# Performance work log

Hardware: AMD Instinct MI355X
Metric: run time of the kernel (lower is better)

The kernel has to match this reference:

```python
import jax, jax.numpy as jnp
import numpy as np

N = 2097152   # total points across all samples
B = 8         # number of point clouds in the batch
C = 64        # feature channels of fea


def setup_inputs() -> dict:
    key = jax.random.key(0)
    k1, k2, k3, k4 = jax.random.split(key, 4)
    fea = jax.random.normal(k1, (N, C), dtype=jnp.float32)
    pred_f = jax.random.normal(k2, (N, 1), dtype=jnp.float32)
    batch_ids = jnp.sort(jax.random.randint(k3, (N,), 0, B).astype(jnp.int32))
    target_points_num = jax.random.randint(k4, (B,), 0, 250000).astype(jnp.int32)
    return {"fea": fea, "pred_f": pred_f, "batch_ids": batch_ids,
            "target_points_num": target_points_num}


def reference(fea, pred_f, batch_ids, target_points_num):
    """BCE branch of GenerativeUpsample.get_keep + feature pruning.

    For each sample b with n_b points and target t_b: if n_b > t_b, threshold is the
    (n_b - t_b)-th smallest pred value (torch.kthvalue, 1-indexed), else dtype min.
    keep = pred > threshold[batch_id]; pruned fea = fea masked by keep.
    """
    vals = pred_f[:, 0]                                  # [N]
    n = vals.shape[0]
    counts = jax.ops.segment_sum(jnp.ones((n,), jnp.int32), batch_ids,
                                 num_segments=B)         # [B] points per sample
    offsets = jnp.concatenate([jnp.zeros((1,), jnp.int32),
                               jnp.cumsum(counts)[:-1].astype(jnp.int32)])
    pos = jnp.arange(n, dtype=jnp.int32) - offsets[batch_ids]  # index within segment

    # Pad each sample's values into a dense row (pad=+inf so pads sort to the end).
    dense = jnp.full((B, n), jnp.inf, dtype=vals.dtype).at[batch_ids, pos].set(vals)
    dense_sorted = jnp.sort(dense, axis=1)               # [B, N]

    # kth smallest (1-indexed k = n_b - t_b) -> sorted index n_b - t_b - 1.
    k_idx = jnp.clip(counts - target_points_num - 1, 0, n - 1)
    kth = jnp.take_along_axis(dense_sorted, k_idx[:, None].astype(jnp.int32), axis=1)[:, 0]
    thresh = jnp.where(counts > target_points_num, kth,
                       jnp.finfo(vals.dtype).min)        # [B]

    keep = vals > thresh[batch_ids]                      # [N] bool
    pruned_fea = fea * keep[:, None].astype(fea.dtype)   # [N, C]
    return pruned_fea, keep
```

## Files before the change

### kernel.cpp

```cpp
#include <hip/hip_runtime.h>
#include <float.h>


#define BATCHES 8

typedef float f32x4 __attribute__((ext_vector_type(4)));

__device__ __forceinline__ unsigned f2key(float x) {
    unsigned u = __float_as_uint(x);
    return (u & 0x80000000u) ? ~u : (u | 0x80000000u);
}
__device__ __forceinline__ float key2f(unsigned k) {
    unsigned u = (k & 0x80000000u) ? (k & 0x7FFFFFFFu) : ~k;
    return __uint_as_float(u);
}

__device__ unsigned g_hist[4 * BATCHES * 256];
__device__ unsigned g_remk[BATCHES];
__device__ unsigned g_prefix[BATCHES];
__device__ unsigned g_active[BATCHES];
__device__ float    g_thresh[BATCHES];

__global__ __launch_bounds__(256) void hist0_kernel(const float* __restrict__ pred,
                                                    const int* __restrict__ bids,
                                                    int n) {
    __shared__ unsigned lh[BATCHES * 256];
    for (int i = threadIdx.x; i < BATCHES * 256; i += 256) lh[i] = 0u;
    __syncthreads();
    int stride = gridDim.x * blockDim.x;
    for (int i = blockIdx.x * blockDim.x + threadIdx.x; i < n; i += stride) {
        int b = bids[i];
        unsigned key = f2key(pred[i]);
        atomicAdd(&lh[b * 256 + (key >> 24)], 1u);
    }
    __syncthreads();
    for (int i = threadIdx.x; i < BATCHES * 256; i += 256) {
        unsigned v = lh[i];
        if (v) atomicAdd(&g_hist[i], v);
    }
}

__global__ __launch_bounds__(256) void histN_kernel(const float* __restrict__ pred,
                                                    const int* __restrict__ bids,
                                                    int n, int shiftHi, int shiftBin,
                                                    int pass) {
    __shared__ unsigned lh[BATCHES * 256];
    __shared__ unsigned lpre[BATCHES];
    __shared__ unsigned lact[BATCHES];
    for (int i = threadIdx.x; i < BATCHES * 256; i += 256) lh[i] = 0u;
    if (threadIdx.x < BATCHES) {
        lpre[threadIdx.x] = g_prefix[threadIdx.x];
        lact[threadIdx.x] = g_active[threadIdx.x];
    }
    __syncthreads();
    int stride = gridDim.x * blockDim.x;
    for (int i = blockIdx.x * blockDim.x + threadIdx.x; i < n; i += stride) {
        int b = bids[i];
        if (!lact[b]) continue;
        unsigned key = f2key(pred[i]);
        if ((key >> shiftHi) == lpre[b])
            atomicAdd(&lh[b * 256 + ((key >> shiftBin) & 0xFFu)], 1u);
    }
    __syncthreads();
    unsigned* gh = g_hist + pass * BATCHES * 256;
    for (int i = threadIdx.x; i < BATCHES * 256; i += 256) {
        unsigned v = lh[i];
        if (v) atomicAdd(&gh[i], v);
    }
}

__global__ __launch_bounds__(256) void scan_kernel(const int* __restrict__ target,
                                                   int pass) {
    int b = blockIdx.x;
    int t = threadIdx.x;
    unsigned* h = g_hist + (pass * BATCHES + b) * 256;
    unsigned c = h[t];
    h[t] = 0u;
    if (pass > 0 && !g_active[b]) {
        if (pass == 3 && t == 0) g_thresh[b] = -FLT_MAX;
        return;
    }
    __shared__ unsigned s[256];
    s[t] = c;
    __syncthreads();
    for (int off = 1; off < 256; off <<= 1) {
        unsigned v = s[t];
        unsigned a = (t >= off) ? s[t - off] : 0u;
        __syncthreads();
        s[t] = v + a;
        __syncthreads();
    }
    unsigned incl = s[t];
    unsigned total = s[255];
    unsigned r;
    if (pass == 0) {
        int tg = target[b];
        bool act = ((int)total > tg) && (total > 0u);
        if (t == 0) g_active[b] = act ? 1u : 0u;
        if (!act) return;
        r = total - (unsigned)tg - 1u;
    } else {
        r = g_remk[b];
    }
    __syncthreads();
    unsigned excl = incl - c;
    if (c > 0u && excl <= r && r < incl) {
        unsigned p = (pass == 0) ? (unsigned)t : ((g_prefix[b] << 8) | (unsigned)t);
        g_prefix[b] = p;
        g_remk[b] = r - excl;
        if (pass == 3) g_thresh[b] = key2f(p);
    }
}

__global__ __launch_bounds__(256) void prune_kernel(const float* __restrict__ fea,
                                                    const float* __restrict__ pred,
                                                    const int* __restrict__ bids,
                                                    float* __restrict__ out,
                                                    int n) {
    __shared__ float sth[BATCHES];
    if (threadIdx.x < BATCHES) sth[threadIdx.x] = g_thresh[threadIdx.x];
    __syncthreads();
    long total4 = (long)n * 16;
    long stride = (long)gridDim.x * blockDim.x;
    for (long idx = (long)blockIdx.x * blockDim.x + threadIdx.x; idx < total4;
         idx += stride) {
        int row = (int)(idx >> 4);
        int l = (int)(idx & 15);
        int b = bids[row];
        bool kp = pred[row] > sth[b];
        f32x4 v = {0.f, 0.f, 0.f, 0.f};
        if (kp) v = __builtin_nontemporal_load((const f32x4*)fea + idx);
        __builtin_nontemporal_store(v, (f32x4*)out + idx);
        if (l == 0) {
            __builtin_nontemporal_store(kp ? 1.0f : 0.0f,
                                        out + (size_t)n * 64 + row);
        }
    }
}

extern "C" void kernel_launch(void* const* d_in, const int* in_sizes, int n_in,
                              void* d_out, int out_size, void* d_ws, size_t ws_size,
                              hipStream_t stream) {
    (void)d_ws; (void)ws_size; (void)n_in; (void)out_size;
    const float* fea    = (const float*)d_in[0];
    const float* pred   = (const float*)d_in[1];
    const int*   bids   = (const int*)d_in[2];
    const int*   target = (const int*)d_in[3];
    float* out = (float*)d_out;
    int n = in_sizes[1];

    hist0_kernel<<<1024, 256, 0, stream>>>(pred, bids, n);
    scan_kernel<<<BATCHES, 256, 0, stream>>>(target, 0);

    for (int p = 1; p <= 3; p++) {
        int shiftHi = 32 - 8 * p;
        int shiftBin = 24 - 8 * p;
        histN_kernel<<<2048, 256, 0, stream>>>(pred, bids, n, shiftHi, shiftBin, p);
        scan_kernel<<<BATCHES, 256, 0, stream>>>(target, p);
    }

    prune_kernel<<<8192, 256, 0, stream>>>(fea, pred, bids, out, n);
}
```

Measured before the change: 908.6 us.

## Fuse radix-select passes and pruning into one cooperative kernel with register-held keys

Replaces the nine-launch pipeline (histogram, scan, three refinement passes, prune) with a single cooperative kernel. Each thread loads its eight pred keys and batch ids once into registers and reuses them across all four radix passes. Grid-wide syncs replace kernel boundaries, and every block redundantly does the per-batch scans with wave shuffles. The trade is grid.sync overhead and a fixed 1024-block grid doing the bandwidth-bound feature copy, with the old path kept as a fallback if the cooperative launch fails.

```diff
diff --git a/kernel.cpp b/kernel.cpp
--- a/kernel.cpp
+++ b/kernel.cpp
@@ -1,8 +1,16 @@
 #include <hip/hip_runtime.h>
+#include <hip/hip_cooperative_groups.h>
 #include <float.h>
 
+namespace cg = cooperative_groups;
+
 
 #define BATCHES 8
+#define NBLK 1024
+#define NTHR 256
+#define NTOT (NBLK * NTHR)
+#define MAXE 8
+#define NEG_FLT_MAX_KEY 0x00800000u
 
 typedef float f32x4 __attribute__((ext_vector_type(4)));
 
@@ -21,6 +29,159 @@
 __device__ unsigned g_active[BATCHES];
 __device__ float    g_thresh[BATCHES];
 
+
+__global__ __launch_bounds__(NTHR, 4) void fused_kernel(
+        const float* __restrict__ fea,
+        const float* __restrict__ pred,
+        const int* __restrict__ bids,
+        const int* __restrict__ target,
+        float* __restrict__ out,
+        int n) {
+    cg::grid_group grid = cg::this_grid();
+    __shared__ unsigned lh[BATCHES * 256];
+    __shared__ unsigned lpre[BATCHES];
+    __shared__ unsigned lremk[BATCHES];
+    __shared__ unsigned lact[BATCHES];
+    __shared__ unsigned lthreshk[BATCHES];
+    __shared__ float    skeep[NTHR];
+
+    const int t = threadIdx.x;
+    const int tid = blockIdx.x * NTHR + t;
+
+    if (blockIdx.x == 0) {
+        for (int i = t; i < 4 * BATCHES * 256; i += NTHR) g_hist[i] = 0u;
+    }
+    for (int i = t; i < BATCHES * 256; i += NTHR) lh[i] = 0u;
+    __syncthreads();
+
+    unsigned key[MAXE];
+    unsigned bn = 0u;
+    #pragma unroll
+    for (int i = 0; i < MAXE; i++) {
+        int idx = tid + i * NTOT;
+        unsigned k = 0u, b = 8u;
+        if (idx < n) {
+            k = f2key(pred[idx]);
+            b = (unsigned)bids[idx];
+            atomicAdd(&lh[b * 256 + (k >> 24)], 1u);
+        }
+        key[i] = k;
+        bn |= (b << (4 * i));
+    }
+    __syncthreads();
+    grid.sync();
+
+    for (int i = t; i < BATCHES * 256; i += NTHR) {
+        unsigned v = lh[i];
+        if (v) atomicAdd(&g_hist[i], v);
+        lh[i] = 0u;
+    }
+    grid.sync();
+
+    #pragma unroll
+    for (int p = 0; p < 4; p++) {
+        {
+            int lane = t & 63;
+            int w = t >> 6;
+            for (int bb = 0; bb < 2; bb++) {
+                int b = w + bb * 4;
+                if (p > 0 && lact[b] == 0u) {
+                    if (p == 3 && lane == 0) lthreshk[b] = NEG_FLT_MAX_KEY;
+                    continue;
+                }
+                const unsigned* h = g_hist + (p * BATCHES + b) * 256;
+                unsigned c0 = h[lane * 4 + 0], c1 = h[lane * 4 + 1];
+                unsigned c2 = h[lane * 4 + 2], c3 = h[lane * 4 + 3];
+                unsigned lt = c0 + c1 + c2 + c3;
+                unsigned sc = lt;
+                #pragma unroll
+                for (int off = 1; off < 64; off <<= 1) {
+                    unsigned u = __shfl_up(sc, off);
+                    if (lane >= off) sc += u;
+                }
+                unsigned total = __shfl(sc, 63);
+                unsigned r;
+                if (p == 0) {
+                    int tg = target[b];
+                    bool act = ((int)total > tg);
+                    if (lane == 0) lact[b] = act ? 1u : 0u;
+                    if (!act) continue;
+                    r = total - (unsigned)tg - 1u;
+                } else {
+                    r = lremk[b];
+                }
+                unsigned excl = sc - lt;
+                if (r >= excl && r < sc) {
+                    unsigned rr = r - excl;
+                    unsigned bin, cum;
+                    if (rr < c0)                { bin = 0u; cum = 0u; }
+                    else if (rr < c0 + c1)      { bin = 1u; cum = c0; }
+                    else if (rr < c0 + c1 + c2) { bin = 2u; cum = c0 + c1; }
+                    else                        { bin = 3u; cum = c0 + c1 + c2; }
+                    unsigned binidx = (unsigned)(lane * 4) + bin;
+                    unsigned np = (p == 0) ? binidx : ((lpre[b] << 8) | binidx);
+                    lpre[b] = np;
+                    lremk[b] = rr - cum;
+                    if (p == 3) lthreshk[b] = np;
+                }
+            }
+        }
+        __syncthreads();
+
+        if (p == 3) break;
+
+        const int shiftHi  = 24 - 8 * p;
+        const int shiftBin = 16 - 8 * p;
+        #pragma unroll
+        for (int i = 0; i < MAXE; i++) {
+            unsigned b = (bn >> (4 * i)) & 0xFu;
+            if (b < 8u && lact[b]) {
+                unsigned k = key[i];
+                if ((k >> shiftHi) == lpre[b])
+                    atomicAdd(&lh[b * 256 + ((k >> shiftBin) & 0xFFu)], 1u);
+            }
+        }
+        __syncthreads();
+        unsigned* gh = g_hist + (p + 1) * BATCHES * 256;
+        for (int i = t; i < BATCHES * 256; i += NTHR) {
+            unsigned v = lh[i];
+            if (v) atomicAdd(&gh[i], v);
+            lh[i] = 0u;
+        }
+        grid.sync();
+    }
+
+    #pragma unroll
+    for (int i = 0; i < MAXE; i++) {
+        int rowbase = blockIdx.x * NTHR + i * NTOT;
+        int idx = rowbase + t;
+        unsigned b = (bn >> (4 * i)) & 0xFu;
+        bool kp = (idx < n) && (b < 8u) && (key[i] > lthreshk[b]);
+        skeep[t] = kp ? 1.0f : 0.0f;
+        __syncthreads();
+        if (rowbase < n) {
+            int rows = min(NTHR, n - rowbase);
+            const f32x4* src = (const f32x4*)fea + (size_t)rowbase * 16;
+            f32x4* dst = (f32x4*)out + (size_t)rowbase * 16;
+            for (int f = t; f < rows * 16; f += NTHR) {
+                int rl = f >> 4;
+                f32x4 v = {0.f, 0.f, 0.f, 0.f};
+                if (skeep[rl] > 0.5f) v = __builtin_nontemporal_load(src + f);
+                __builtin_nontemporal_store(v, dst + f);
+            }
+            if (idx < n)
+                __builtin_nontemporal_store(skeep[t], out + (size_t)n * 64 + idx);
+        }
+        __syncthreads();
+    }
+}
+
+
+__global__ void zero_hist_kernel() {
+    int i = blockIdx.x * blockDim.x + threadIdx.x;
+    if (i < 4 * BATCHES * 256) g_hist[i] = 0u;
+}
+
 __global__ __launch_bounds__(256) void hist0_kernel(const float* __restrict__ pred,
                                                     const int* __restrict__ bids,
                                                     int n) {
@@ -30,8 +191,8 @@
     int stride = gridDim.x * blockDim.x;
     for (int i = blockIdx.x * blockDim.x + threadIdx.x; i < n; i += stride) {
         int b = bids[i];
-        unsigned key = f2key(pred[i]);
-        atomicAdd(&lh[b * 256 + (key >> 24)], 1u);
+        unsigned k = f2key(pred[i]);
+        atomicAdd(&lh[b * 256 + (k >> 24)], 1u);
     }
     __syncthreads();
     for (int i = threadIdx.x; i < BATCHES * 256; i += 256) {
@@ -57,9 +218,9 @@
     for (int i = blockIdx.x * blockDim.x + threadIdx.x; i < n; i += stride) {
         int b = bids[i];
         if (!lact[b]) continue;
-        unsigned key = f2key(pred[i]);
-        if ((key >> shiftHi) == lpre[b])
-            atomicAdd(&lh[b * 256 + ((key >> shiftBin) & 0xFFu)], 1u);
+        unsigned k = f2key(pred[i]);
+        if ((k >> shiftHi) == lpre[b])
+            atomicAdd(&lh[b * 256 + ((k >> shiftBin) & 0xFFu)], 1u);
     }
     __syncthreads();
     unsigned* gh = g_hist + pass * BATCHES * 256;
@@ -131,12 +292,11 @@
         f32x4 v = {0.f, 0.f, 0.f, 0.f};
         if (kp) v = __builtin_nontemporal_load((const f32x4*)fea + idx);
         __builtin_nontemporal_store(v, (f32x4*)out + idx);
-        if (l == 0) {
-            __builtin_nontemporal_store(kp ? 1.0f : 0.0f,
-                                        out + (size_t)n * 64 + row);
-        }
-    }
-}
+        if (l == 0)
+            __builtin_nontemporal_store(kp ? 1.0f : 0.0f, out + (size_t)n * 64 + row);
+    }
+}
+
 
 extern "C" void kernel_launch(void* const* d_in, const int* in_sizes, int n_in,
                               void* d_out, int out_size, void* d_ws, size_t ws_size,
@@ -149,15 +309,23 @@
     float* out = (float*)d_out;
     int n = in_sizes[1];
 
-    hist0_kernel<<<1024, 256, 0, stream>>>(pred, bids, n);
-    scan_kernel<<<BATCHES, 256, 0, stream>>>(target, 0);
-
-    for (int p = 1; p <= 3; p++) {
-        int shiftHi = 32 - 8 * p;
-        int shiftBin = 24 - 8 * p;
-        histN_kernel<<<2048, 256, 0, stream>>>(pred, bids, n, shiftHi, shiftBin, p);
-        scan_kernel<<<BATCHES, 256, 0, stream>>>(target, p);
-    }
-
-    prune_kernel<<<8192, 256, 0, stream>>>(fea, pred, bids, out, n);
-}
+    hipError_t e = hipErrorUnknown;
+    if (n <= NTOT * MAXE) {
+        void* args[] = {(void*)&fea, (void*)&pred, (void*)&bids,
+                        (void*)&target, (void*)&out, (void*)&n};
+        e = hipLaunchCooperativeKernel(reinterpret_cast<void*>(fused_kernel),
+                                       dim3(NBLK), dim3(NTHR), args, 0, stream);
+    }
+    if (e != hipSuccess) {
+        zero_hist_kernel<<<32, 256, 0, stream>>>();
+        hist0_kernel<<<1024, 256, 0, stream>>>(pred, bids, n);
+        scan_kernel<<<BATCHES, 256, 0, stream>>>(target, 0);
+        for (int p = 1; p <= 3; p++) {
+            int shiftHi = 32 - 8 * p;
+            int shiftBin = 24 - 8 * p;
+            histN_kernel<<<2048, 256, 0, stream>>>(pred, bids, n, shiftHi, shiftBin, p);
+            scan_kernel<<<BATCHES, 256, 0, stream>>>(target, p);
+        }
+        prune_kernel<<<8192, 256, 0, stream>>>(fea, pred, bids, out, n);
+    }
+}
```

Result: slower. 1.380 ms (+51.9%).
